# Kernel optimization log

Measured on AMD Instinct MI355X. Metric: run time of the kernel, lower is better.

The kernel has to match this reference:

```python
import jax, jax.numpy as jnp
import numpy as np

N_NODES = 50000
N_EDGES = 800000


def _gat_conv(x, src, dst, n, W, a_src, a_dst, b, concat):
    # x: [N, Fin]; W: [Fin, H*C]; a_src/a_dst: [H, C]; b: [H*C] or [C]
    H, C = a_src.shape
    h = (x @ W).reshape(n, H, C)                     # [N,H,C]
    alpha_src = jnp.sum(h * a_src[None], axis=-1)    # [N,H]
    alpha_dst = jnp.sum(h * a_dst[None], axis=-1)    # [N,H]
    e = alpha_src[src] + alpha_dst[dst]              # [E,H]
    e = jax.nn.leaky_relu(e, negative_slope=0.2)
    # segment softmax over incoming edges of each dst node
    m = jax.ops.segment_max(e, dst, num_segments=n)  # [N,H]
    ex = jnp.exp(e - m[dst])
    s = jax.ops.segment_sum(ex, dst, num_segments=n)
    alpha = ex / (s[dst] + 1e-16)                    # [E,H]
    msg = h[src] * alpha[:, :, None]                 # [E,H,C]
    out = jax.ops.segment_sum(msg, dst, num_segments=n)  # [N,H,C]
    out = out.reshape(n, H * C) if concat else out.mean(axis=1)
    return out + b


def setup_inputs() -> dict:
    key = jax.random.key(0)
    ks = jax.random.split(key, 12)
    d = {}
    d['x'] = jax.random.normal(ks[0], (N_NODES, 128), dtype=jnp.float32)
    d['edge_index'] = jax.random.randint(ks[1], (2, N_EDGES), 0, N_NODES, dtype=jnp.int32)
    s = 0.1
    d['w1'] = jax.random.normal(ks[2], (128, 128), dtype=jnp.float32) * s
    d['att_src1'] = jax.random.normal(ks[3], (2, 64), dtype=jnp.float32) * s
    d['att_dst1'] = jax.random.normal(ks[4], (2, 64), dtype=jnp.float32) * s
    d['b1'] = jnp.zeros((128,), jnp.float32)
    d['w2'] = jax.random.normal(ks[5], (128, 128), dtype=jnp.float32) * s
    d['att_src2'] = jax.random.normal(ks[6], (2, 64), dtype=jnp.float32) * s
    d['att_dst2'] = jax.random.normal(ks[7], (2, 64), dtype=jnp.float32) * s
    d['b2'] = jnp.zeros((128,), jnp.float32)
    d['w3'] = jax.random.normal(ks[8], (128, 40), dtype=jnp.float32) * s
    d['att_src3'] = jax.random.normal(ks[9], (1, 40), dtype=jnp.float32) * s
    d['att_dst3'] = jax.random.normal(ks[10], (1, 40), dtype=jnp.float32) * s
    d['b3'] = jnp.zeros((40,), jnp.float32)
    return d


def reference(x, edge_index, w1, att_src1, att_dst1, b1,
              w2, att_src2, att_dst2, b2, w3, att_src3, att_dst3, b3):
    n = x.shape[0]
    # PyG GATConv adds self-loops by default
    loop = jnp.arange(n, dtype=edge_index.dtype)
    src = jnp.concatenate([edge_index[0], loop])
    dst = jnp.concatenate([edge_index[1], loop])
    h = _gat_conv(x, src, dst, n, w1, att_src1, att_dst1, b1, concat=True)
    h = jax.nn.elu(h)  # dropout skipped (eval mode)
    h = _gat_conv(h, src, dst, n, w2, att_src2, att_dst2, b2, concat=True)
    h = jax.nn.elu(h)
    out = _gat_conv(h, src, dst, n, w3, att_src3, att_dst3, b3, concat=False)
    return out
```

## Files before the change

### kernel.cpp

```cpp
#include <hip/hip_runtime.h>
#include <hip/hip_fp16.h>

#define NN 50000
#define NE 800000
#define E2 850000
#define SCAN_NB 49
#define GEMM_BLKS 782
#define P_CH 128
#define CH 6641
#define HWORDS 12500
#define COLS_BLKS 98

static inline int cdiv(long long a, int b) { return (int)((a + b - 1) / b); }

using half8  = __attribute__((ext_vector_type(8))) _Float16;
using floatx4 = __attribute__((ext_vector_type(4))) float;

struct __align__(16) h2x4 { __half2 a, b, c, d; };
struct __align__(8)  h2x2 { __half2 a, b; };

__device__ __forceinline__ void edge_sd(const int* __restrict__ ei, int e, int& s, int& d) {
    if (e < NE) { s = ei[e]; d = ei[NE + e]; }
    else { s = e - NE; d = s; }
}

__device__ __forceinline__ half8 cvt_h8(float4 a, float4 b) {
    half8 r;
    r[0] = (_Float16)a.x; r[1] = (_Float16)a.y; r[2] = (_Float16)a.z; r[3] = (_Float16)a.w;
    r[4] = (_Float16)b.x; r[5] = (_Float16)b.y; r[6] = (_Float16)b.z; r[7] = (_Float16)b.w;
    return r;
}

__global__ __launch_bounds__(512) void hist_rank(const int* __restrict__ ei,
                                                 unsigned* __restrict__ cnt,
                                                 unsigned short* __restrict__ rank16) {
    __shared__ unsigned hist[HWORDS];
    const int c = blockIdx.x >> 1;
    const int hf = blockIdx.x & 1;
    const int tid = threadIdx.x;
    for (int i = tid; i < HWORDS; i += 512) hist[i] = 0;
    __syncthreads();
    const int e0 = c * CH;
    const int e1 = (e0 + CH < E2) ? e0 + CH : E2;
    const int wlo = hf * HWORDS;
    for (int e = e0 + tid; e < e1; e += 512) {
        int d = (e < NE) ? ei[NE + e] : (e - NE);
        int w = (d >> 1) - wlo;
        if ((unsigned)w < HWORDS) {
            unsigned sh = (d & 1) * 16;
            unsigned old = atomicAdd(&hist[w], 1u << sh);
            rank16[e] = (unsigned short)((old >> sh) & 0xffffu);
        }
    }
    __syncthreads();
    unsigned* dst = &cnt[(size_t)c * 25000 + wlo];
    for (int i = tid; i < HWORDS; i += 512) dst[i] = hist[i];
}

__global__ __launch_bounds__(256) void colscan(const unsigned* __restrict__ cnt,
                                               unsigned* __restrict__ chunkbase,
                                               int* __restrict__ deg,
                                               int* __restrict__ ctr,
                                               const float* __restrict__ w1, __half* __restrict__ wt1,
                                               const float* __restrict__ w2, __half* __restrict__ wt2,
                                               const float* __restrict__ w3, __half* __restrict__ wt3) {
    int b = blockIdx.x;
    if (b < COLS_BLKS) {
        if (b == 0 && threadIdx.x == 0) *ctr = 0;
        int w = b * 256 + threadIdx.x;
        if (w >= 25000) return;
        unsigned run = 0;
#pragma unroll 4
        for (int c = 0; c < P_CH; ++c) {
            unsigned r = cnt[(size_t)c * 25000 + w];
            chunkbase[(size_t)c * 25000 + w] = run;
            run += r;
        }
        deg[2 * w]     = (int)(run & 0xffffu);
        deg[2 * w + 1] = (int)(run >> 16);
        return;
    }
    int tid = (b - COLS_BLKS) * 256 + threadIdx.x;
    int stride = (gridDim.x - COLS_BLKS) * 256;
    for (int i = tid; i < 128 * 128; i += stride)
        wt1[i] = __float2half(w1[(i & 127) * 128 + (i >> 7)]);
    for (int i = tid; i < 128 * 128; i += stride)
        wt2[i] = __float2half(w2[(i & 127) * 128 + (i >> 7)]);
    for (int i = tid; i < 40 * 128; i += stride)
        wt3[i] = __float2half(w3[(i & 127) * 40 + (i >> 7)]);
}

__global__ __launch_bounds__(256) void scan_all(const int* __restrict__ deg,
                                                int* __restrict__ rowp,
                                                int* __restrict__ bsums,
                                                int* __restrict__ ctr) {
    __shared__ int wsum[4];
    __shared__ int sh_pref[64];
    int tid = threadIdx.x;
    int base = blockIdx.x * 1024 + tid * 4;
    int4 v = make_int4(0, 0, 0, 0);
    if (base + 3 < NN) v = *(const int4*)&deg[base];
    else {
        if (base + 0 < NN) v.x = deg[base + 0];
        if (base + 1 < NN) v.y = deg[base + 1];
        if (base + 2 < NN) v.z = deg[base + 2];
    }
    v.y += v.x; v.z += v.y; v.w += v.z;
    int lane = tid & 63;
    int wid = tid >> 6;
    int t = v.w;
#pragma unroll
    for (int off = 1; off < 64; off <<= 1) {
        int u = __shfl_up(t, off, 64);
        if (lane >= off) t += u;
    }
    int excl = t - v.w;
    if (lane == 63) wsum[wid] = t;
    __syncthreads();
    int woff = 0;
    for (int w = 0; w < wid; ++w) woff += wsum[w];
    int add = excl + woff;
    if (tid == 255) {
        bsums[blockIdx.x] = add + v.w;
        __threadfence();
        atomicAdd(ctr, 1);
    }
    if (tid == 0) {
        while (__hip_atomic_load(ctr, __ATOMIC_ACQUIRE, __HIP_MEMORY_SCOPE_AGENT) < SCAN_NB) {
            __builtin_amdgcn_s_sleep(8);
        }
    }
    __syncthreads();
    if (tid < 64) {
        int bv = (tid < SCAN_NB)
            ? __hip_atomic_load(&bsums[tid], __ATOMIC_RELAXED, __HIP_MEMORY_SCOPE_AGENT) : 0;
        int s = bv;
#pragma unroll
        for (int off = 1; off < 64; off <<= 1) {
            int u = __shfl_up(s, off, 64);
            if (tid >= off) s += u;
        }
        sh_pref[tid] = s - bv;
    }
    __syncthreads();
    int boff = sh_pref[blockIdx.x];
    if (base == 0) rowp[0] = 0;
    if (base + 0 < NN) rowp[base + 1] = v.x + add + boff;
    if (base + 1 < NN) rowp[base + 2] = v.y + add + boff;
    if (base + 2 < NN) rowp[base + 3] = v.z + add + boff;
    if (base + 3 < NN) rowp[base + 4] = v.w + add + boff;
}

template<int MOUT, int H, bool XF32>
__device__ __forceinline__ void gemm_body(int bid, const void* __restrict__ Xv,
                                          const __half* __restrict__ WT,
                                          const float* __restrict__ aS,
                                          const float* __restrict__ aD,
                                          __half* __restrict__ Ho,
                                          float* __restrict__ osrc,
                                          float* __restrict__ odst,
                                          __half* wlds) {
    constexpr int NT = (MOUT + 15) / 16;
    constexpr int NR = NT * 16;
    const int tid = threadIdx.x;
    for (int i = tid * 8; i < MOUT * 128; i += 2048) {
        half8 v = *(const half8*)&WT[i];
        *(half8*)&wlds[(i >> 7) * 136 + (i & 127)] = v;
    }
    if (NR > MOUT) {
        for (int i = tid * 8; i < (NR - MOUT) * 128; i += 2048) {
            half8 z = {};
            *(half8*)&wlds[(MOUT + (i >> 7)) * 136 + (i & 127)] = z;
        }
    }
    __syncthreads();

    const int lane = tid & 63;
    const int wid = tid >> 6;
    const int r0 = bid * 64 + wid * 16;
    const int arow = r0 + (lane & 15);
    const int lrow = (arow < NN) ? arow : (NN - 1);
    const int koff = (lane >> 4) * 8;
    half8 a0, a1, a2, a3;
    if constexpr (XF32) {
        const float* Xf = (const float*)Xv;
        const size_t xb = (size_t)lrow * 128 + koff;
        a0 = cvt_h8(*(const float4*)&Xf[xb +  0], *(const float4*)&Xf[xb +  4]);
        a1 = cvt_h8(*(const float4*)&Xf[xb + 32], *(const float4*)&Xf[xb + 36]);
        a2 = cvt_h8(*(const float4*)&Xf[xb + 64], *(const float4*)&Xf[xb + 68]);
        a3 = cvt_h8(*(const float4*)&Xf[xb + 96], *(const float4*)&Xf[xb + 100]);
    } else {
        const __half* Xh = (const __half*)Xv;
        const size_t xb = (size_t)lrow * 128 + koff;
        a0 = *(const half8*)&Xh[xb];
        a1 = *(const half8*)&Xh[xb + 32];
        a2 = *(const half8*)&Xh[xb + 64];
        a3 = *(const half8*)&Xh[xb + 96];
    }

    floatx4 acc[NT];
#pragma unroll
    for (int t = 0; t < NT; ++t) acc[t] = (floatx4){0.f, 0.f, 0.f, 0.f};

#pragma unroll
    for (int t = 0; t < NT; ++t) {
        const __half* wp = &wlds[(t * 16 + (lane & 15)) * 136 + koff];
        half8 b0 = *(const half8*)&wp[0];
        half8 b1 = *(const half8*)&wp[32];
        half8 b2 = *(const half8*)&wp[64];
        half8 b3 = *(const half8*)&wp[96];
        acc[t] = __builtin_amdgcn_mfma_f32_16x16x32_f16(a0, b0, acc[t], 0, 0, 0);
        acc[t] = __builtin_amdgcn_mfma_f32_16x16x32_f16(a1, b1, acc[t], 0, 0, 0);
        acc[t] = __builtin_amdgcn_mfma_f32_16x16x32_f16(a2, b2, acc[t], 0, 0, 0);
        acc[t] = __builtin_amdgcn_mfma_f32_16x16x32_f16(a3, b3, acc[t], 0, 0, 0);
    }

    const int cc = lane & 15;
    const int rbase = r0 + (lane >> 4) * 4;
    float ps[H][4], pd[H][4];
#pragma unroll
    for (int h = 0; h < H; ++h)
#pragma unroll
        for (int r = 0; r < 4; ++r) { ps[h][r] = 0.f; pd[h][r] = 0.f; }

#pragma unroll
    for (int t = 0; t < NT; ++t) {
        const int col = t * 16 + cc;
        const bool cv = (col < MOUT);
        const float as_ = cv ? aS[col] : 0.f;
        const float ad_ = cv ? aD[col] : 0.f;
        const int h = (H == 2) ? (t >> 2) : 0;
#pragma unroll
        for (int r = 0; r < 4; ++r) {
            ps[h][r] = fmaf(acc[t][r], as_, ps[h][r]);
            pd[h][r] = fmaf(acc[t][r], ad_, pd[h][r]);
        }
    }

    if constexpr (MOUT == 128) {
        __syncthreads();
        const int rowbase = wid * 16;
#pragma unroll
        for (int t = 0; t < NT; ++t)
#pragma unroll
            for (int r = 0; r < 4; ++r)
                wlds[(rowbase + (lane >> 4) * 4 + r) * 136 + t * 16 + cc] =
                    __float2half(acc[t][r]);
        __syncthreads();
#pragma unroll
        for (int p2 = 0; p2 < 4; ++p2) {
            int f = (p2 * 64 + lane) * 8;
            int row = f >> 7, col = f & 127;
            h2x4 v = *(h2x4*)&wlds[(rowbase + row) * 136 + col];
            int grow = r0 + row;
            if (grow < NN) *(h2x4*)&Ho[(size_t)grow * 128 + col] = v;
        }
    } else {
#pragma unroll
        for (int t = 0; t < NT; ++t) {
            const int col = t * 16 + cc;
            const bool cv = (col < MOUT);
#pragma unroll
            for (int r = 0; r < 4; ++r) {
                const int m = rbase + r;
                if (cv && m < NN) Ho[(size_t)m * MOUT + col] = __float2half(acc[t][r]);
            }
        }
    }

#pragma unroll
    for (int off = 1; off <= 8; off <<= 1) {
#pragma unroll
        for (int h = 0; h < H; ++h)
#pragma unroll
            for (int r = 0; r < 4; ++r) {
                ps[h][r] += __shfl_xor(ps[h][r], off, 64);
                pd[h][r] += __shfl_xor(pd[h][r], off, 64);
            }
    }
    if (cc == 0) {
#pragma unroll
        for (int r = 0; r < 4; ++r) {
            const int m = rbase + r;
            if (m < NN) {
#pragma unroll
                for (int h = 0; h < H; ++h) {
                    osrc[m * H + h] = ps[h][r];
                    odst[m * H + h] = pd[h][r];
                }
            }
        }
    }
}

__global__ __launch_bounds__(256) void gemm16_k128(const __half* __restrict__ X,
                                                   const __half* __restrict__ WT,
                                                   const float* __restrict__ aS,
                                                   const float* __restrict__ aD,
                                                   __half* __restrict__ Ho,
                                                   float* __restrict__ osrc,
                                                   float* __restrict__ odst) {
    __shared__ __half wlds[128 * 136];
    gemm_body<128, 2, false>(blockIdx.x, X, WT, aS, aD, Ho, osrc, odst, wlds);
}

__global__ __launch_bounds__(256) void gemm16_k40(const __half* __restrict__ X,
                                                  const __half* __restrict__ WT,
                                                  const float* __restrict__ aS,
                                                  const float* __restrict__ aD,
                                                  __half* __restrict__ Ho,
                                                  float* __restrict__ osrc,
                                                  float* __restrict__ odst) {
    __shared__ __half wlds[48 * 136];
    gemm_body<40, 1, false>(blockIdx.x, X, WT, aS, aD, Ho, osrc, odst, wlds);
}

__global__ __launch_bounds__(256) void gemm1_scat(const float* __restrict__ X,
                                                  const __half* __restrict__ WT,
                                                  const float* __restrict__ aS,
                                                  const float* __restrict__ aD,
                                                  __half* __restrict__ Ho,
                                                  float* __restrict__ osrc,
                                                  float* __restrict__ odst,
                                                  const int* __restrict__ ei,
                                                  const int* __restrict__ rowp,
                                                  const unsigned short* __restrict__ rank16,
                                                  const unsigned* __restrict__ chunkbase,
                                                  int* __restrict__ csr_src) {
    __shared__ __half wlds[128 * 136];
    if (blockIdx.x < GEMM_BLKS) {
        gemm_body<128, 2, true>(blockIdx.x, X, WT, aS, aD, Ho, osrc, odst, wlds);
        return;
    }
    int e = (blockIdx.x - GEMM_BLKS) * 256 + threadIdx.x;
    if (e >= E2) return;
    int c = e / CH;
    int s, d; edge_sd(ei, e, s, d);
    unsigned cb = chunkbase[(size_t)c * 25000 + (d >> 1)];
    int off = (int)((cb >> ((d & 1) * 16)) & 0xffffu);
    csr_src[rowp[d] + off + (int)rank16[e]] = s;
}

__global__ __launch_bounds__(256) void agg_h2(const int* __restrict__ rowp,
                                              const int* __restrict__ csr_src,
                                              const __half* __restrict__ Hf,
                                              const float* __restrict__ osrc,
                                              const float* __restrict__ odst,
                                              const float* __restrict__ bias,
                                              __half* __restrict__ outp) {
    int n = blockIdx.x * 4 + (threadIdx.x >> 6);
    if (n >= NN) return;
    int lane = threadIdx.x & 63;
    int i0 = rowp[n], i1 = rowp[n + 1];
    int c = lane & 15;
    int slot = lane >> 4;
    int c8 = c * 8;
    int h2 = c >> 3;
    float adh = odst[n * 2 + h2];
    bool pl = ((c & 7) == 0);

    float4 lo0{0.f,0.f,0.f,0.f}, hi0{0.f,0.f,0.f,0.f};
    float4 lo1{0.f,0.f,0.f,0.f}, hi1{0.f,0.f,0.f,0.f};
    float psum = 0.f;

    int idx = i0 + slot;
    for (; idx + 12 < i1; idx += 16) {
        int s0 = csr_src[idx];
        int s1 = csr_src[idx + 4];
        int s2 = csr_src[idx + 8];
        int s3 = csr_src[idx + 12];
        float e0 = osrc[s0 * 2 + h2] + adh;
        float e1 = osrc[s1 * 2 + h2] + adh;
        float e2 = osrc[s2 * 2 + h2] + adh;
        float e3 = osrc[s3 * 2 + h2] + adh;
        e0 = (e0 >= 0.f) ? e0 : 0.2f * e0;
        e1 = (e1 >= 0.f) ? e1 : 0.2f * e1;
        e2 = (e2 >= 0.f) ? e2 : 0.2f * e2;
        e3 = (e3 >= 0.f) ? e3 : 0.2f * e3;
        float p0 = __expf(e0), p1 = __expf(e1), p2 = __expf(e2), p3 = __expf(e3);
        h2x4 hv0 = *(const h2x4*)&Hf[(size_t)s0 * 128 + c8];
        h2x4 hv1 = *(const h2x4*)&Hf[(size_t)s1 * 128 + c8];
        h2x4 hv2 = *(const h2x4*)&Hf[(size_t)s2 * 128 + c8];
        h2x4 hv3 = *(const h2x4*)&Hf[(size_t)s3 * 128 + c8];
        if (pl) psum += (p0 + p1) + (p2 + p3);
        float2 f;
        f = __half22float2(hv0.a); lo0.x = fmaf(f.x, p0, lo0.x); lo0.y = fmaf(f.y, p0, lo0.y);
        f = __half22float2(hv0.b); lo0.z = fmaf(f.x, p0, lo0.z); lo0.w = fmaf(f.y, p0, lo0.w);
        f = __half22float2(hv0.c); hi0.x = fmaf(f.x, p0, hi0.x); hi0.y = fmaf(f.y, p0, hi0.y);
        f = __half22float2(hv0.d); hi0.z = fmaf(f.x, p0, hi0.z); hi0.w = fmaf(f.y, p0, hi0.w);
        f = __half22float2(hv1.a); lo0.x = fmaf(f.x, p1, lo0.x); lo0.y = fmaf(f.y, p1, lo0.y);
        f = __half22float2(hv1.b); lo0.z = fmaf(f.x, p1, lo0.z); lo0.w = fmaf(f.y, p1, lo0.w);
        f = __half22float2(hv1.c); hi0.x = fmaf(f.x, p1, hi0.x); hi0.y = fmaf(f.y, p1, hi0.y);
        f = __half22float2(hv1.d); hi0.z = fmaf(f.x, p1, hi0.z); hi0.w = fmaf(f.y, p1, hi0.w);
        f = __half22float2(hv2.a); lo1.x = fmaf(f.x, p2, lo1.x); lo1.y = fmaf(f.y, p2, lo1.y);
        f = __half22float2(hv2.b); lo1.z = fmaf(f.x, p2, lo1.z); lo1.w = fmaf(f.y, p2, lo1.w);
        f = __half22float2(hv2.c); hi1.x = fmaf(f.x, p2, hi1.x); hi1.y = fmaf(f.y, p2, hi1.y);
        f = __half22float2(hv2.d); hi1.z = fmaf(f.x, p2, hi1.z); hi1.w = fmaf(f.y, p2, hi1.w);
        f = __half22float2(hv3.a); lo1.x = fmaf(f.x, p3, lo1.x); lo1.y = fmaf(f.y, p3, lo1.y);
        f = __half22float2(hv3.b); lo1.z = fmaf(f.x, p3, lo1.z); lo1.w = fmaf(f.y, p3, lo1.w);
        f = __half22float2(hv3.c); hi1.x = fmaf(f.x, p3, hi1.x); hi1.y = fmaf(f.y, p3, hi1.y);
        f = __half22float2(hv3.d); hi1.z = fmaf(f.x, p3, hi1.z); hi1.w = fmaf(f.y, p3, hi1.w);
    }
    {
        int id1 = idx + 4, id2 = idx + 8;
        bool v0 = idx < i1, v1 = id1 < i1, v2 = id2 < i1;
        int lim = i1 - 1;
        int s0 = csr_src[min(idx, lim)];
        int s1 = csr_src[min(id1, lim)];
        int s2 = csr_src[min(id2, lim)];
        float e0 = osrc[s0 * 2 + h2] + adh;
        float e1 = osrc[s1 * 2 + h2] + adh;
        float e2 = osrc[s2 * 2 + h2] + adh;
        e0 = (e0 >= 0.f) ? e0 : 0.2f * e0;
        e1 = (e1 >= 0.f) ? e1 : 0.2f * e1;
        e2 = (e2 >= 0.f) ? e2 : 0.2f * e2;
        float p0 = v0 ? __expf(e0) : 0.f;
        float p1 = v1 ? __expf(e1) : 0.f;
        float p2 = v2 ? __expf(e2) : 0.f;
        h2x4 hv0 = *(const h2x4*)&Hf[(size_t)s0 * 128 + c8];
        h2x4 hv1 = *(const h2x4*)&Hf[(size_t)s1 * 128 + c8];
        h2x4 hv2 = *(const h2x4*)&Hf[(size_t)s2 * 128 + c8];
        if (pl) psum += (p0 + p1) + p2;
        float2 f;
        f = __half22float2(hv0.a); lo0.x = fmaf(f.x, p0, lo0.x); lo0.y = fmaf(f.y, p0, lo0.y);
        f = __half22float2(hv0.b); lo0.z = fmaf(f.x, p0, lo0.z); lo0.w = fmaf(f.y, p0, lo0.w);
        f = __half22float2(hv0.c); hi0.x = fmaf(f.x, p0, hi0.x); hi0.y = fmaf(f.y, p0, hi0.y);
        f = __half22float2(hv0.d); hi0.z = fmaf(f.x, p0, hi0.z); hi0.w = fmaf(f.y, p0, hi0.w);
        f = __half22float2(hv1.a); lo0.x = fmaf(f.x, p1, lo0.x); lo0.y = fmaf(f.y, p1, lo0.y);
        f = __half22float2(hv1.b); lo0.z = fmaf(f.x, p1, lo0.z); lo0.w = fmaf(f.y, p1, lo0.w);
        f = __half22float2(hv1.c); hi0.x = fmaf(f.x, p1, hi0.x); hi0.y = fmaf(f.y, p1, hi0.y);
        f = __half22float2(hv1.d); hi0.z = fmaf(f.x, p1, hi0.z); hi0.w = fmaf(f.y, p1, hi0.w);
        f = __half22float2(hv2.a); lo1.x = fmaf(f.x, p2, lo1.x); lo1.y = fmaf(f.y, p2, lo1.y);
        f = __half22float2(hv2.b); lo1.z = fmaf(f.x, p2, lo1.z); lo1.w = fmaf(f.y, p2, lo1.w);
        f = __half22float2(hv2.c); hi1.x = fmaf(f.x, p2, hi1.x); hi1.y = fmaf(f.y, p2, hi1.y);
        f = __half22float2(hv2.d); hi1.z = fmaf(f.x, p2, hi1.z); hi1.w = fmaf(f.y, p2, hi1.w);
    }
    float4 lo{lo0.x + lo1.x, lo0.y + lo1.y, lo0.z + lo1.z, lo0.w + lo1.w};
    float4 hi{hi0.x + hi1.x, hi0.y + hi1.y, hi0.z + hi1.z, hi0.w + hi1.w};
#pragma unroll
    for (int off = 16; off <= 32; off <<= 1) {
        lo.x += __shfl_xor(lo.x, off, 64); lo.y += __shfl_xor(lo.y, off, 64);
        lo.z += __shfl_xor(lo.z, off, 64); lo.w += __shfl_xor(lo.w, off, 64);
        hi.x += __shfl_xor(hi.x, off, 64); hi.y += __shfl_xor(hi.y, off, 64);
        hi.z += __shfl_xor(hi.z, off, 64); hi.w += __shfl_xor(hi.w, off, 64);
        psum += __shfl_xor(psum, off, 64);
    }
    float sh = __shfl(psum, h2 * 8, 64);
    float inv = 1.f / (sh + 1e-16f);
    if (lane < 16) {
        float4 bl = *(const float4*)&bias[c8];
        float4 bh = *(const float4*)&bias[c8 + 4];
        float o0 = fmaf(lo.x, inv, bl.x), o1 = fmaf(lo.y, inv, bl.y);
        float o2 = fmaf(lo.z, inv, bl.z), o3 = fmaf(lo.w, inv, bl.w);
        float o4 = fmaf(hi.x, inv, bh.x), o5 = fmaf(hi.y, inv, bh.y);
        float o6 = fmaf(hi.z, inv, bh.z), o7 = fmaf(hi.w, inv, bh.w);
        o0 = (o0 > 0.f) ? o0 : (__expf(o0) - 1.f);
        o1 = (o1 > 0.f) ? o1 : (__expf(o1) - 1.f);
        o2 = (o2 > 0.f) ? o2 : (__expf(o2) - 1.f);
        o3 = (o3 > 0.f) ? o3 : (__expf(o3) - 1.f);
        o4 = (o4 > 0.f) ? o4 : (__expf(o4) - 1.f);
        o5 = (o5 > 0.f) ? o5 : (__expf(o5) - 1.f);
        o6 = (o6 > 0.f) ? o6 : (__expf(o6) - 1.f);
        o7 = (o7 > 0.f) ? o7 : (__expf(o7) - 1.f);
        h2x4 st;
        st.a = __floats2half2_rn(o0, o1);
        st.b = __floats2half2_rn(o2, o3);
        st.c = __floats2half2_rn(o4, o5);
        st.d = __floats2half2_rn(o6, o7);
        *(h2x4*)&outp[(size_t)n * 128 + c8] = st;
    }
}

__global__ __launch_bounds__(256) void agg_h1(const int* __restrict__ rowp,
                                              const int* __restrict__ csr_src,
                                              const __half* __restrict__ Hf,
                                              const float* __restrict__ osrc,
                                              const float* __restrict__ odst,
                                              const float* __restrict__ bias,
                                              float* __restrict__ outp) {
    int n = blockIdx.x * 4 + (threadIdx.x >> 6);
    if (n >= NN) return;
    int lane = threadIdx.x & 63;
    int i0 = rowp[n], i1 = rowp[n + 1];
    float ad = odst[n];
    int c = lane & 15;
    int slot = lane >> 4;
    bool cl = (c < 10);
    bool pl = (c == 0);
    float4 acc0{0.f,0.f,0.f,0.f}, acc1{0.f,0.f,0.f,0.f};
    float psum = 0.f;

    int idx = i0 + slot;
    for (; idx + 12 < i1; idx += 16) {
        int s0 = csr_src[idx];
        int s1 = csr_src[idx + 4];
        int s2 = csr_src[idx + 8];
        int s3 = csr_src[idx + 12];
        float e0 = osrc[s0] + ad, e1 = osrc[s1] + ad;
        float e2 = osrc[s2] + ad, e3 = osrc[s3] + ad;
        e0 = (e0 >= 0.f) ? e0 : 0.2f * e0;
        e1 = (e1 >= 0.f) ? e1 : 0.2f * e1;
        e2 = (e2 >= 0.f) ? e2 : 0.2f * e2;
        e3 = (e3 >= 0.f) ? e3 : 0.2f * e3;
        float p0 = __expf(e0), p1 = __expf(e1), p2 = __expf(e2), p3 = __expf(e3);
        if (pl) psum += (p0 + p1) + (p2 + p3);
        if (cl) {
            h2x2 hv0 = *(const h2x2*)&Hf[(size_t)s0 * 40 + c * 4];
            h2x2 hv1 = *(const h2x2*)&Hf[(size_t)s1 * 40 + c * 4];
            h2x2 hv2 = *(const h2x2*)&Hf[(size_t)s2 * 40 + c * 4];
            h2x2 hv3 = *(const h2x2*)&Hf[(size_t)s3 * 40 + c * 4];
            float2 f;
            f = __half22float2(hv0.a); acc0.x = fmaf(f.x, p0, acc0.x); acc0.y = fmaf(f.y, p0, acc0.y);
            f = __half22float2(hv0.b); acc0.z = fmaf(f.x, p0, acc0.z); acc0.w = fmaf(f.y, p0, acc0.w);
            f = __half22float2(hv1.a); acc1.x = fmaf(f.x, p1, acc1.x); acc1.y = fmaf(f.y, p1, acc1.y);
            f = __half22float2(hv1.b); acc1.z = fmaf(f.x, p1, acc1.z); acc1.w = fmaf(f.y, p1, acc1.w);
            f = __half22float2(hv2.a); acc0.x = fmaf(f.x, p2, acc0.x); acc0.y = fmaf(f.y, p2, acc0.y);
            f = __half22float2(hv2.b); acc0.z = fmaf(f.x, p2, acc0.z); acc0.w = fmaf(f.y, p2, acc0.w);
            f = __half22float2(hv3.a); acc1.x = fmaf(f.x, p3, acc1.x); acc1.y = fmaf(f.y, p3, acc1.y);
            f = __half22float2(hv3.b); acc1.z = fmaf(f.x, p3, acc1.z); acc1.w = fmaf(f.y, p3, acc1.w);
        }
    }
    {
        int id1 = idx + 4, id2 = idx + 8;
        bool v0 = idx < i1, v1 = id1 < i1, v2 = id2 < i1;
        int lim = i1 - 1;
        int s0 = csr_src[min(idx, lim)];
        int s1 = csr_src[min(id1, lim)];
        int s2 = csr_src[min(id2, lim)];
        float e0 = osrc[s0] + ad, e1 = osrc[s1] + ad, e2 = osrc[s2] + ad;
        e0 = (e0 >= 0.f) ? e0 : 0.2f * e0;
        e1 = (e1 >= 0.f) ? e1 : 0.2f * e1;
        e2 = (e2 >= 0.f) ? e2 : 0.2f * e2;
        float p0 = v0 ? __expf(e0) : 0.f;
        float p1 = v1 ? __expf(e1) : 0.f;
        float p2 = v2 ? __expf(e2) : 0.f;
        if (pl) psum += (p0 + p1) + p2;
        if (cl) {
            h2x2 hv0 = *(const h2x2*)&Hf[(size_t)s0 * 40 + c * 4];
            h2x2 hv1 = *(const h2x2*)&Hf[(size_t)s1 * 40 + c * 4];
            h2x2 hv2 = *(const h2x2*)&Hf[(size_t)s2 * 40 + c * 4];
            float2 f;
            f = __half22float2(hv0.a); acc0.x = fmaf(f.x, p0, acc0.x); acc0.y = fmaf(f.y, p0, acc0.y);
            f = __half22float2(hv0.b); acc0.z = fmaf(f.x, p0, acc0.z); acc0.w = fmaf(f.y, p0, acc0.w);
            f = __half22float2(hv1.a); acc1.x = fmaf(f.x, p1, acc1.x); acc1.y = fmaf(f.y, p1, acc1.y);
            f = __half22float2(hv1.b); acc1.z = fmaf(f.x, p1, acc1.z); acc1.w = fmaf(f.y, p1, acc1.w);
            f = __half22float2(hv2.a); acc0.x = fmaf(f.x, p2, acc0.x); acc0.y = fmaf(f.y, p2, acc0.y);
            f = __half22float2(hv2.b); acc0.z = fmaf(f.x, p2, acc0.z); acc0.w = fmaf(f.y, p2, acc0.w);
        }
    }
    float4 acc{acc0.x + acc1.x, acc0.y + acc1.y, acc0.z + acc1.z, acc0.w + acc1.w};
#pragma unroll
    for (int off = 16; off <= 32; off <<= 1) {
        acc.x += __shfl_xor(acc.x, off, 64);
        acc.y += __shfl_xor(acc.y, off, 64);
        acc.z += __shfl_xor(acc.z, off, 64);
        acc.w += __shfl_xor(acc.w, off, 64);
        psum += __shfl_xor(psum, off, 64);
    }
    float sh = __shfl(psum, 0, 64);
    float inv = 1.f / (sh + 1e-16f);
    if (lane < 10) {
        float4 b = *(const float4*)&bias[lane * 4];
        float4 o;
        o.x = fmaf(acc.x, inv, b.x);
        o.y = fmaf(acc.y, inv, b.y);
        o.z = fmaf(acc.z, inv, b.z);
        o.w = fmaf(acc.w, inv, b.w);
        *(float4*)&outp[(size_t)n * 40 + lane * 4] = o;
    }
}

extern "C" void kernel_launch(void* const* d_in, const int* in_sizes, int n_in,
                              void* d_out, int out_size, void* d_ws, size_t ws_size,
                              hipStream_t stream) {
    const float* x   = (const float*)d_in[0];
    const int*   ei  = (const int*)d_in[1];
    const float* w1  = (const float*)d_in[2];
    const float* as1 = (const float*)d_in[3];
    const float* ad1 = (const float*)d_in[4];
    const float* b1  = (const float*)d_in[5];
    const float* w2  = (const float*)d_in[6];
    const float* as2 = (const float*)d_in[7];
    const float* ad2 = (const float*)d_in[8];
    const float* b2  = (const float*)d_in[9];
    const float* w3  = (const float*)d_in[10];
    const float* as3 = (const float*)d_in[11];
    const float* ad3 = (const float*)d_in[12];
    const float* b3  = (const float*)d_in[13];
    float* out = (float*)d_out;

    char* p = (char*)d_ws;
    __half*   h16    = (__half*)p;   p += (size_t)NN * 128 * 2;
    __half*   f16    = (__half*)p;   p += (size_t)NN * 128 * 2;
    unsigned* cnt    = (unsigned*)p; p += (size_t)P_CH * 25000 * 4;
    unsigned* cbase  = (unsigned*)p; p += (size_t)P_CH * 25000 * 4;
    __half*   wt1    = (__half*)p;   p += (size_t)128 * 128 * 2;
    __half*   wt2    = (__half*)p;   p += (size_t)128 * 128 * 2;
    __half*   wt3    = (__half*)p;   p += (size_t)64 * 128 * 2;
    float*    osrc   = (float*)p;    p += (size_t)NN * 2 * 4;
    float*    odst   = (float*)p;    p += (size_t)NN * 2 * 4;
    int*      rowp   = (int*)p;      p += (size_t)(NN + 4) * 4;
    int*      deg    = (int*)p;      p += (size_t)NN * 4;
    unsigned short* rank16 = (unsigned short*)p; p += (size_t)E2 * 2;
    int*      bsums  = (int*)p;      p += (size_t)64 * 4;
    int*      ctr    = (int*)p;      p += (size_t)4 * 4;
    int*      csrsrc = (int*)p;      p += (size_t)E2 * 4;

    const int edgeGrid = cdiv(E2, 256);
    const int nodeGrid = cdiv(NN, 4);

    hist_rank<<<P_CH * 2, 512, 0, stream>>>(ei, cnt, rank16);
    colscan<<<COLS_BLKS + 64, 256, 0, stream>>>(cnt, cbase, deg, ctr,
                                                w1, wt1, w2, wt2, w3, wt3);
    scan_all<<<SCAN_NB, 256, 0, stream>>>(deg, rowp, bsums, ctr);

    gemm1_scat<<<GEMM_BLKS + edgeGrid, 256, 0, stream>>>(x, wt1, as1, ad1, h16,
                                                         osrc, odst, ei, rowp,
                                                         rank16, cbase, csrsrc);
    agg_h2<<<nodeGrid, 256, 0, stream>>>(rowp, csrsrc, h16, osrc, odst, b1, f16);

    gemm16_k128<<<GEMM_BLKS, 256, 0, stream>>>(f16, wt2, as2, ad2, h16, osrc, odst);
    agg_h2<<<nodeGrid, 256, 0, stream>>>(rowp, csrsrc, h16, osrc, odst, b2, f16);

    gemm16_k40<<<GEMM_BLKS, 256, 0, stream>>>(f16, wt3, as3, ad3, h16, osrc, odst);
    agg_h1<<<nodeGrid, 256, 0, stream>>>(rowp, csrsrc, h16, osrc, odst, b3, out);
}
```

Before: 183.7 us.

## Fuse column scan and row-pointer scan into one kernel with in-place chunk bases

Merges the per-chunk column prefix kernel and the global degree scan into a single kernel. Each block scans its 512 node degrees, publishes a block sum, and waits on an atomic counter spin barrier before adding the prefix of earlier blocks. The chunk bases are now written back into the count buffer in place, which drops the separate chunkbase and deg buffers, and the counter reset moves into hist_rank. This saves one kernel launch and some global traffic, but relies on all 98 scan blocks being co-resident alongside the weight-conversion blocks for the spin barrier.

```diff
diff --git a/kernel.cpp b/kernel.cpp
--- a/kernel.cpp
+++ b/kernel.cpp
@@ -4,7 +4,6 @@
 #define NN 50000
 #define NE 800000
 #define E2 850000
-#define SCAN_NB 49
 #define GEMM_BLKS 782
 #define P_CH 128
 #define CH 6641
@@ -33,11 +32,13 @@
 
 __global__ __launch_bounds__(512) void hist_rank(const int* __restrict__ ei,
                                                  unsigned* __restrict__ cnt,
-                                                 unsigned short* __restrict__ rank16) {
+                                                 unsigned short* __restrict__ rank16,
+                                                 int* __restrict__ ctr) {
     __shared__ unsigned hist[HWORDS];
     const int c = blockIdx.x >> 1;
     const int hf = blockIdx.x & 1;
     const int tid = threadIdx.x;
+    if (blockIdx.x == 0 && tid == 0) *ctr = 0;
     for (int i = tid; i < HWORDS; i += 512) hist[i] = 0;
     __syncthreads();
     const int e0 = c * CH;
@@ -57,27 +58,73 @@
     for (int i = tid; i < HWORDS; i += 512) dst[i] = hist[i];
 }
 
-__global__ __launch_bounds__(256) void colscan(const unsigned* __restrict__ cnt,
-                                               unsigned* __restrict__ chunkbase,
-                                               int* __restrict__ deg,
-                                               int* __restrict__ ctr,
-                                               const float* __restrict__ w1, __half* __restrict__ wt1,
-                                               const float* __restrict__ w2, __half* __restrict__ wt2,
-                                               const float* __restrict__ w3, __half* __restrict__ wt3) {
+__global__ __launch_bounds__(256) void cscan(unsigned* __restrict__ cnt,
+                                             int* __restrict__ rowp,
+                                             int* __restrict__ bsums,
+                                             int* __restrict__ ctr,
+                                             const float* __restrict__ w1, __half* __restrict__ wt1,
+                                             const float* __restrict__ w2, __half* __restrict__ wt2,
+                                             const float* __restrict__ w3, __half* __restrict__ wt3) {
     int b = blockIdx.x;
     if (b < COLS_BLKS) {
-        if (b == 0 && threadIdx.x == 0) *ctr = 0;
-        int w = b * 256 + threadIdx.x;
-        if (w >= 25000) return;
+        __shared__ int wsum[4];
+        __shared__ int shb[128];
+        __shared__ int bb_s;
+        int tid = threadIdx.x;
+        int w = b * 256 + tid;
         unsigned run = 0;
+        if (w < 25000) {
 #pragma unroll 4
-        for (int c = 0; c < P_CH; ++c) {
-            unsigned r = cnt[(size_t)c * 25000 + w];
-            chunkbase[(size_t)c * 25000 + w] = run;
-            run += r;
-        }
-        deg[2 * w]     = (int)(run & 0xffffu);
-        deg[2 * w + 1] = (int)(run >> 16);
+            for (int c = 0; c < P_CH; ++c) {
+                unsigned r = cnt[(size_t)c * 25000 + w];
+                cnt[(size_t)c * 25000 + w] = run;
+                run += r;
+            }
+        }
+        int lo = (int)(run & 0xffffu);
+        int hi = (int)(run >> 16);
+        int tot = lo + hi;
+        int lane = tid & 63, wid = tid >> 6;
+        int t = tot;
+#pragma unroll
+        for (int off = 1; off < 64; off <<= 1) {
+            int u = __shfl_up(t, off, 64);
+            if (lane >= off) t += u;
+        }
+        int excl = t - tot;
+        if (lane == 63) wsum[wid] = t;
+        __syncthreads();
+        int woff = 0;
+        for (int ww = 0; ww < wid; ++ww) woff += wsum[ww];
+        excl += woff;
+        if (tid == 255) {
+            bsums[b] = excl + tot;
+            __threadfence();
+            atomicAdd(ctr, 1);
+        }
+        if (tid == 0) {
+            while (__hip_atomic_load(ctr, __ATOMIC_ACQUIRE, __HIP_MEMORY_SCOPE_AGENT) < COLS_BLKS) {
+                __builtin_amdgcn_s_sleep(8);
+            }
+        }
+        __syncthreads();
+        if (tid < 128)
+            shb[tid] = (tid < b) ?
+                __hip_atomic_load(&bsums[tid], __ATOMIC_RELAXED, __HIP_MEMORY_SCOPE_AGENT) : 0;
+        __syncthreads();
+        if (tid < 64) {
+            int v = shb[tid] + shb[tid + 64];
+#pragma unroll
+            for (int off = 32; off >= 1; off >>= 1) v += __shfl_xor(v, off, 64);
+            if (tid == 0) bb_s = v;
+        }
+        __syncthreads();
+        int bb = bb_s;
+        if (b == 0 && tid == 0) rowp[0] = 0;
+        if (w < 25000) {
+            rowp[2 * w + 1] = bb + excl + lo;
+            rowp[2 * w + 2] = bb + excl + lo + hi;
+        }
         return;
     }
     int tid = (b - COLS_BLKS) * 256 + threadIdx.x;
@@ -88,67 +135,6 @@
         wt2[i] = __float2half(w2[(i & 127) * 128 + (i >> 7)]);
     for (int i = tid; i < 40 * 128; i += stride)
         wt3[i] = __float2half(w3[(i & 127) * 40 + (i >> 7)]);
-}
-
-__global__ __launch_bounds__(256) void scan_all(const int* __restrict__ deg,
-                                                int* __restrict__ rowp,
-                                                int* __restrict__ bsums,
-                                                int* __restrict__ ctr) {
-    __shared__ int wsum[4];
-    __shared__ int sh_pref[64];
-    int tid = threadIdx.x;
-    int base = blockIdx.x * 1024 + tid * 4;
-    int4 v = make_int4(0, 0, 0, 0);
-    if (base + 3 < NN) v = *(const int4*)&deg[base];
-    else {
-        if (base + 0 < NN) v.x = deg[base + 0];
-        if (base + 1 < NN) v.y = deg[base + 1];
-        if (base + 2 < NN) v.z = deg[base + 2];
-    }
-    v.y += v.x; v.z += v.y; v.w += v.z;
-    int lane = tid & 63;
-    int wid = tid >> 6;
-    int t = v.w;
-#pragma unroll
-    for (int off = 1; off < 64; off <<= 1) {
-        int u = __shfl_up(t, off, 64);
-        if (lane >= off) t += u;
-    }
-    int excl = t - v.w;
-    if (lane == 63) wsum[wid] = t;
-    __syncthreads();
-    int woff = 0;
-    for (int w = 0; w < wid; ++w) woff += wsum[w];
-    int add = excl + woff;
-    if (tid == 255) {
-        bsums[blockIdx.x] = add + v.w;
-        __threadfence();
-        atomicAdd(ctr, 1);
-    }
-    if (tid == 0) {
-        while (__hip_atomic_load(ctr, __ATOMIC_ACQUIRE, __HIP_MEMORY_SCOPE_AGENT) < SCAN_NB) {
-            __builtin_amdgcn_s_sleep(8);
-        }
-    }
-    __syncthreads();
-    if (tid < 64) {
-        int bv = (tid < SCAN_NB)
-            ? __hip_atomic_load(&bsums[tid], __ATOMIC_RELAXED, __HIP_MEMORY_SCOPE_AGENT) : 0;
-        int s = bv;
-#pragma unroll
-        for (int off = 1; off < 64; off <<= 1) {
-            int u = __shfl_up(s, off, 64);
-            if (tid >= off) s += u;
-        }
-        sh_pref[tid] = s - bv;
-    }
-    __syncthreads();
-    int boff = sh_pref[blockIdx.x];
-    if (base == 0) rowp[0] = 0;
-    if (base + 0 < NN) rowp[base + 1] = v.x + add + boff;
-    if (base + 1 < NN) rowp[base + 2] = v.y + add + boff;
-    if (base + 2 < NN) rowp[base + 3] = v.z + add + boff;
-    if (base + 3 < NN) rowp[base + 4] = v.w + add + boff;
 }
 
 template<int MOUT, int H, bool XF32>
@@ -593,30 +579,27 @@
     __half*   h16    = (__half*)p;   p += (size_t)NN * 128 * 2;
     __half*   f16    = (__half*)p;   p += (size_t)NN * 128 * 2;
     unsigned* cnt    = (unsigned*)p; p += (size_t)P_CH * 25000 * 4;
-    unsigned* cbase  = (unsigned*)p; p += (size_t)P_CH * 25000 * 4;
     __half*   wt1    = (__half*)p;   p += (size_t)128 * 128 * 2;
     __half*   wt2    = (__half*)p;   p += (size_t)128 * 128 * 2;
     __half*   wt3    = (__half*)p;   p += (size_t)64 * 128 * 2;
     float*    osrc   = (float*)p;    p += (size_t)NN * 2 * 4;
     float*    odst   = (float*)p;    p += (size_t)NN * 2 * 4;
     int*      rowp   = (int*)p;      p += (size_t)(NN + 4) * 4;
-    int*      deg    = (int*)p;      p += (size_t)NN * 4;
     unsigned short* rank16 = (unsigned short*)p; p += (size_t)E2 * 2;
-    int*      bsums  = (int*)p;      p += (size_t)64 * 4;
+    int*      bsums  = (int*)p;      p += (size_t)128 * 4;
     int*      ctr    = (int*)p;      p += (size_t)4 * 4;
     int*      csrsrc = (int*)p;      p += (size_t)E2 * 4;
 
     const int edgeGrid = cdiv(E2, 256);
     const int nodeGrid = cdiv(NN, 4);
 
-    hist_rank<<<P_CH * 2, 512, 0, stream>>>(ei, cnt, rank16);
-    colscan<<<COLS_BLKS + 64, 256, 0, stream>>>(cnt, cbase, deg, ctr,
-                                                w1, wt1, w2, wt2, w3, wt3);
-    scan_all<<<SCAN_NB, 256, 0, stream>>>(deg, rowp, bsums, ctr);
+    hist_rank<<<P_CH * 2, 512, 0, stream>>>(ei, cnt, rank16, ctr);
+    cscan<<<COLS_BLKS + 64, 256, 0, stream>>>(cnt, rowp, bsums, ctr,
+                                              w1, wt1, w2, wt2, w3, wt3);
 
     gemm1_scat<<<GEMM_BLKS + edgeGrid, 256, 0, stream>>>(x, wt1, as1, ad1, h16,
                                                          osrc, odst, ei, rowp,
-                                                         rank16, cbase, csrsrc);
+                                                         rank16, cnt, csrsrc);
     agg_h2<<<nodeGrid, 256, 0, stream>>>(rowp, csrsrc, h16, osrc, odst, b1, f16);
 
     gemm16_k128<<<GEMM_BLKS, 256, 0, stream>>>(f16, wt2, as2, ad2, h16, osrc, odst);
```

After: 184.3 us. No clear change (+0.3%).
